# Kernel optimization log

Hardware: AMD Instinct MI355X
Metric: run time of the kernel (lower is better)

## Reference

```python
import jax, jax.numpy as jnp
import numpy as np

D_MODEL = 1024
H = 16
D_K = D_MODEL // H
B, S = 2, 2048
NEG = -1.0e9


def setup_inputs() -> dict:
    key = jax.random.key(0)
    ks = jax.random.split(key, 9)
    sc = 1.0 / np.sqrt(D_MODEL)
    x = jax.random.normal(ks[0], (B, S, D_MODEL), dtype=jnp.float32)
    mask = jnp.tril(jnp.ones((S, S), dtype=jnp.int32))[None, None]  # causal [1,1,S,S]
    Wq = jax.random.normal(ks[1], (D_MODEL, D_MODEL), jnp.float32) * sc
    bq = jnp.zeros((D_MODEL,), jnp.float32)
    Wk = jax.random.normal(ks[2], (D_MODEL, D_MODEL), jnp.float32) * sc
    bk = jnp.zeros((D_MODEL,), jnp.float32)
    Wv = jax.random.normal(ks[3], (D_MODEL, D_MODEL), jnp.float32) * sc
    bv = jnp.zeros((D_MODEL,), jnp.float32)
    Wo = jax.random.normal(ks[4], (D_MODEL, D_MODEL), jnp.float32) * sc
    bo = jnp.zeros((D_MODEL,), jnp.float32)
    return {"x": x, "mask": mask, "Wq": Wq, "bq": bq, "Wk": Wk, "bk": bk,
            "Wv": Wv, "bv": bv, "Wo": Wo, "bo": bo}


def reference(x, mask, Wq, bq, Wk, bk, Wv, bv, Wo, bo):
    Bx, Sx, _ = x.shape
    # QKV projections (nn.Linear: x @ W.T + b)
    q = (x @ Wq.T + bq).reshape(Bx, Sx, H, D_K).transpose(0, 2, 1, 3)  # [B,h,S,dk]
    k = (x @ Wk.T + bk).reshape(Bx, Sx, H, D_K).transpose(0, 2, 1, 3)
    v = (x @ Wv.T + bv).reshape(Bx, Sx, H, D_K).transpose(0, 2, 1, 3)
    scores = jnp.einsum('bhqd,bhkd->bhqk', q, k) / np.sqrt(D_K)  # [B,h,S,S]
    scores = jnp.where(mask == 0, NEG, scores)
    attn = jax.nn.softmax(scores, axis=-1)  # dropout p=0 -> identity
    out = jnp.einsum('bhqk,bhkd->bhqd', attn, v)
    out = out.transpose(0, 2, 1, 3).reshape(Bx, Sx, H * D_K)
    return out @ Wo.T + bo
```

## Files before the change

### kernel.cpp

```cpp
#include <hip/hip_runtime.h>
#include <hip/hip_bf16.h>

typedef __bf16 bf16;
typedef bf16 bf16x8 __attribute__((ext_vector_type(8)));
typedef bf16 bf16x4 __attribute__((ext_vector_type(4)));
typedef float f32x4 __attribute__((ext_vector_type(4)));
typedef float f32x16 __attribute__((ext_vector_type(16)));
typedef unsigned int u32;
typedef u32 u32x4 __attribute__((ext_vector_type(4)));

#define S_LEN 2048
#define DM 1024
#define NH 16
#define DK 64
#define MTOK 4096

__device__ __forceinline__ void gld16(const void* g, void* l) {
  __builtin_amdgcn_global_load_lds(
      (const __attribute__((address_space(1))) u32*)g,
      (__attribute__((address_space(3))) u32*)l, 16, 0, 0);
}

__device__ __forceinline__ u32 pkbf(float lo, float hi) {
  union { bf16 h[2]; u32 u; } c;
  c.h[0] = (bf16)lo; c.h[1] = (bf16)hi;
  return c.u;
}
__device__ __forceinline__ void plswap(u32& a, u32& b) {
  asm volatile("v_permlane32_swap_b32 %0, %1" : "+v"(a), "+v"(b));
}

__global__ __launch_bounds__(256) void cvt_all(
    const float* __restrict__ x, const float* __restrict__ wq, const float* __restrict__ wk,
    const float* __restrict__ wv, const float* __restrict__ wo,
    bf16* __restrict__ xb, bf16* __restrict__ wqb, bf16* __restrict__ wkb,
    bf16* __restrict__ wvb, bf16* __restrict__ wob) {
  const int i = blockIdx.x * blockDim.x + threadIdx.x;
  const int NX = (MTOK * DM) / 4;
  const int NW = (DM * DM) / 4;
  const float* src;
  bf16* dst;
  int off;
  if (i < NX) {
    src = x; dst = xb; off = i;
  } else {
    const int j = i - NX;
    const int w = j >> 18;
    off = j & (NW - 1);
    src = (w == 0) ? wq : (w == 1) ? wk : (w == 2) ? wv : wo;
    dst = (w == 0) ? wqb : (w == 1) ? wkb : (w == 2) ? wvb : wob;
  }
  f32x4 v = reinterpret_cast<const f32x4*>(src)[off];
  bf16x4 o;
  o[0] = (bf16)v[0]; o[1] = (bf16)v[1]; o[2] = (bf16)v[2]; o[3] = (bf16)v[3];
  reinterpret_cast<bf16x4*>(dst)[off] = o;
}

__global__ __launch_bounds__(256) void gemm_qkv(
    const bf16* __restrict__ A,
    const bf16* __restrict__ Wq, const bf16* __restrict__ Wk, const bf16* __restrict__ Wv,
    const float* __restrict__ Bq, const float* __restrict__ Bk, const float* __restrict__ Bv,
    bf16* __restrict__ Qo, bf16* __restrict__ Ko, bf16* __restrict__ Vt) {
  __shared__ char smem[65536];
  const int z = blockIdx.z;
  const bf16* W = (z == 0) ? Wq : (z == 1) ? Wk : Wv;
  const float* bias = (z == 0) ? Bq : (z == 1) ? Bk : Bv;
  const int m0 = blockIdx.y * 128;
  const int n0 = blockIdx.x * 128;
  const int tid = threadIdx.x;
  const int lane = tid & 63;
  const int wid = tid >> 6;
  const int wr = (wid >> 1) * 64, wc = (wid & 1) * 64;
  const int scb = 16 * ((lane & 7) ^ (lane >> 3));
  const int lr8 = lane >> 3;

  f32x4 acc[4][4] = {};

  auto STAGE = [&](int bi, int k0) {
#pragma unroll
    for (int c = 0; c < 4; ++c) {
      const int chunk = wid * 4 + c;
      const int row = chunk * 8 + lr8;
      gld16((const char*)A + ((size_t)(m0 + row) * DM + k0) * 2 + scb,
            smem + bi * 32768 + chunk * 1024);
      gld16((const char*)W + ((size_t)(n0 + row) * DM + k0) * 2 + scb,
            smem + bi * 32768 + 16384 + chunk * 1024);
    }
  };

  STAGE(0, 0);
  asm volatile("s_waitcnt vmcnt(0)" ::: "memory");
  __builtin_amdgcn_s_barrier();

  const int NK = DM / 64;
  for (int it = 0; it < NK; ++it) {
    if (it + 1 < NK) STAGE((it + 1) & 1, (it + 1) * 64);
    const char* As = smem + (it & 1) * 32768;
    const char* Bs = As + 16384;
#pragma unroll
    for (int kk = 0; kk < 2; ++kk) {
      bf16x8 af[4], bfr[4];
#pragma unroll
      for (int i = 0; i < 4; ++i) {
        const int ar = wr + i * 16 + (lane & 15);
        af[i] = *reinterpret_cast<const bf16x8*>(
            As + ar * 128 + ((kk * 64 + 16 * (lane >> 4)) ^ ((ar & 7) << 4)));
        const int br = wc + i * 16 + (lane & 15);
        bfr[i] = *reinterpret_cast<const bf16x8*>(
            Bs + br * 128 + ((kk * 64 + 16 * (lane >> 4)) ^ ((br & 7) << 4)));
      }
      __builtin_amdgcn_s_setprio(1);
#pragma unroll
      for (int i = 0; i < 4; ++i)
#pragma unroll
        for (int j = 0; j < 4; ++j)
          acc[i][j] = __builtin_amdgcn_mfma_f32_16x16x32_bf16(af[i], bfr[j], acc[i][j], 0, 0, 0);
      __builtin_amdgcn_s_setprio(0);
    }
    asm volatile("s_waitcnt vmcnt(0)" ::: "memory");
    __builtin_amdgcn_s_barrier();
  }

  const float QSC = 0.125f * 1.44269504089f;
  const int bIdx = m0 >> 11;
  const int r4 = (lane >> 4) * 4;
#pragma unroll
  for (int i = 0; i < 4; ++i) {
    const int mrow = m0 + wr + i * 16 + r4;
    const int srow = mrow & (S_LEN - 1);
#pragma unroll
    for (int j = 0; j < 4; ++j) {
      const int n = n0 + wc + j * 16 + (lane & 15);
      const int h = n >> 6, d = n & 63;
      const int bh = bIdx * NH + h;
      const float bs = bias[n];
      if (z == 0) {
#pragma unroll
        for (int r = 0; r < 4; ++r)
          Qo[((size_t)bh * S_LEN + srow + r) * DK + d] = (bf16)((acc[i][j][r] + bs) * QSC);
      } else if (z == 1) {
#pragma unroll
        for (int r = 0; r < 4; ++r)
          Ko[((size_t)bh * S_LEN + srow + r) * DK + d] = (bf16)(acc[i][j][r] + bs);
      } else {
        bf16x4 pk;
#pragma unroll
        for (int r = 0; r < 4; ++r) pk[r] = (bf16)(acc[i][j][r] + bs);
        *reinterpret_cast<bf16x4*>(&Vt[((size_t)bh * DK + d) * S_LEN + srow]) = pk;
      }
    }
  }
}

__global__ __launch_bounds__(256) void attn_fwd(
    const bf16* __restrict__ Q, const bf16* __restrict__ K,
    const bf16* __restrict__ Vt, bf16* __restrict__ O) {
  __shared__ char smem[49152];

  const int bid = blockIdx.x;
  const int qt = 15 - (bid >> 5);
  const int bh = bid & 31;
  const int tid = threadIdx.x, lane = tid & 63, wid = tid >> 6;
  const int q0 = qt * 128;
  const int scb = 16 * ((lane & 7) ^ (lane >> 3));
  const int l31 = lane & 31;
  const int hi = lane >> 5;
  const int qrow = q0 + wid * 32 + l31;
  const int swz = (l31 & 7) << 4;

  const bf16* qb = Q + ((size_t)bh * S_LEN + qrow) * DK;
  bf16x8 qf[4];
#pragma unroll
  for (int ks = 0; ks < 4; ++ks)
    qf[ks] = *reinterpret_cast<const bf16x8*>(qb + ks * 16 + 8 * hi);

  f32x16 o0 = {}, o1 = {};
  float m_r = -3.0e38f, l_r = 0.f;

  const int nt = 2 * (qt + 1);

  auto STAGE = [&](int bi, int t) {
    const int kv0 = t * 64;
#pragma unroll
    for (int c = 0; c < 2; ++c) {
      const int chunk = wid * 2 + c;
      const int row = chunk * 8 + (lane >> 3);
      gld16((const char*)K + ((size_t)(bh * S_LEN + kv0 + row)) * 128 + scb,
            smem + bi * 16384 + chunk * 1024);
      gld16((const char*)Vt + ((size_t)(bh * DK + row)) * (S_LEN * 2) + (size_t)kv0 * 2 + scb,
            smem + bi * 16384 + 8192 + chunk * 1024);
    }
  };

  STAGE(0, 0);

  for (int t = 0; t < nt; ++t) {
    const int kv0 = t * 64;
    if (t + 1 < nt) {
      STAGE((t + 1) % 3, t + 1);
      asm volatile("s_waitcnt vmcnt(4)" ::: "memory");
    } else {
      asm volatile("s_waitcnt vmcnt(0)" ::: "memory");
    }
    __builtin_amdgcn_s_barrier();
    asm volatile("" ::: "memory");
    const char* Kc = smem + (t % 3) * 16384;
    const char* Vc = Kc + 8192;

    f32x16 s0 = {}, s1 = {};
#pragma unroll
    for (int kt = 0; kt < 2; ++kt) {
      bf16x8 ka[4];
#pragma unroll
      for (int ks = 0; ks < 4; ++ks)
        ka[ks] = *reinterpret_cast<const bf16x8*>(
            Kc + (kt * 32 + l31) * 128 + ((ks * 32 + 16 * hi) ^ swz));
      f32x16& sd = kt ? s1 : s0;
      __builtin_amdgcn_s_setprio(1);
#pragma unroll
      for (int ks = 0; ks < 4; ++ks)
        sd = __builtin_amdgcn_mfma_f32_32x32x16_bf16(ka[ks], qf[ks], sd, 0, 0, 0);
      __builtin_amdgcn_s_setprio(0);
    }

    if (t >= nt - 2) {
#pragma unroll
      for (int r = 0; r < 16; ++r) {
        const int key0 = kv0 + (r & 3) + 8 * (r >> 2) + 4 * hi;
        if (key0 > qrow) s0[r] = -1.0e9f;
        if (key0 + 32 > qrow) s1[r] = -1.0e9f;
      }
    }

    float mx = s0[0];
#pragma unroll
    for (int r = 1; r < 16; ++r) mx = fmaxf(mx, s0[r]);
#pragma unroll
    for (int r = 0; r < 16; ++r) mx = fmaxf(mx, s1[r]);
    mx = fmaxf(mx, __shfl_xor(mx, 32));
    if (!__all(mx <= m_r + 8.f)) {
      const float nm = fmaxf(m_r, mx);
      const float sc = exp2f(m_r - nm);
      l_r *= sc;
      o0 *= sc;
      o1 *= sc;
      m_r = nm;
    }
    float rs = 0.f;
#pragma unroll
    for (int r = 0; r < 16; ++r) { s0[r] = exp2f(s0[r] - m_r); rs += s0[r]; }
#pragma unroll
    for (int r = 0; r < 16; ++r) { s1[r] = exp2f(s1[r] - m_r); rs += s1[r]; }
    rs += __shfl_xor(rs, 32);
    l_r += rs;

    bf16x8 pb[4];
#pragma unroll
    for (int kt = 0; kt < 2; ++kt) {
      const f32x16& p = kt ? s1 : s0;
#pragma unroll
      for (int s2 = 0; s2 < 2; ++s2) {
        u32 cA = pkbf(p[8 * s2 + 0], p[8 * s2 + 1]);
        u32 cB = pkbf(p[8 * s2 + 2], p[8 * s2 + 3]);
        u32 cC = pkbf(p[8 * s2 + 4], p[8 * s2 + 5]);
        u32 cD = pkbf(p[8 * s2 + 6], p[8 * s2 + 7]);
        plswap(cA, cC);
        plswap(cB, cD);
        u32x4 w;
        w[0] = cA; w[1] = cB; w[2] = cC; w[3] = cD;
        pb[kt * 2 + s2] = __builtin_bit_cast(bf16x8, w);
      }
    }

#pragma unroll
    for (int dt = 0; dt < 2; ++dt) {
      bf16x8 va[4];
#pragma unroll
      for (int ks = 0; ks < 4; ++ks)
        va[ks] = *reinterpret_cast<const bf16x8*>(
            Vc + (dt * 32 + l31) * 128 + ((ks * 32 + 16 * hi) ^ swz));
      f32x16& od = dt ? o1 : o0;
      __builtin_amdgcn_s_setprio(1);
#pragma unroll
      for (int ks = 0; ks < 4; ++ks)
        od = __builtin_amdgcn_mfma_f32_32x32x16_bf16(va[ks], pb[ks], od, 0, 0, 0);
      __builtin_amdgcn_s_setprio(0);
    }
  }

  const int b = bh >> 4, h = bh & 15;
  const float inv = 1.0f / l_r;
  bf16* obase = O + ((size_t)(b * S_LEN + qrow)) * DM + h * DK;
#pragma unroll
  for (int dt = 0; dt < 2; ++dt) {
    const f32x16& od = dt ? o1 : o0;
#pragma unroll
    for (int g = 0; g < 4; ++g) {
      bf16x4 pk4;
#pragma unroll
      for (int m = 0; m < 4; ++m) pk4[m] = (bf16)(od[4 * g + m] * inv);
      *reinterpret_cast<bf16x4*>(obase + dt * 32 + 8 * g + 4 * hi) = pk4;
    }
  }
}

__global__ __launch_bounds__(256) void gemm_out(
    const bf16* __restrict__ A, const bf16* __restrict__ W,
    const float* __restrict__ bias, float* __restrict__ C) {
  __shared__ char smem[65536];
  const int m0 = blockIdx.y * 128, n0 = blockIdx.x * 128;
  const int tid = threadIdx.x, lane = tid & 63, wid = tid >> 6;
  const int wr = (wid >> 1) * 64, wc = (wid & 1) * 64;
  const int scb = 16 * ((lane & 7) ^ (lane >> 3));
  const int lr8 = lane >> 3;
  f32x4 acc[4][4] = {};

  auto STAGE = [&](int bi, int k0) {
#pragma unroll
    for (int c = 0; c < 4; ++c) {
      const int chunk = wid * 4 + c;
      const int row = chunk * 8 + lr8;
      gld16((const char*)A + ((size_t)(m0 + row) * DM + k0) * 2 + scb,
            smem + bi * 32768 + chunk * 1024);
      gld16((const char*)W + ((size_t)(n0 + row) * DM + k0) * 2 + scb,
            smem + bi * 32768 + 16384 + chunk * 1024);
    }
  };

  STAGE(0, 0);
  asm volatile("s_waitcnt vmcnt(0)" ::: "memory");
  __builtin_amdgcn_s_barrier();

  const int NK = DM / 64;
  for (int it = 0; it < NK; ++it) {
    if (it + 1 < NK) STAGE((it + 1) & 1, (it + 1) * 64);
    const char* As = smem + (it & 1) * 32768;
    const char* Bs = As + 16384;
#pragma unroll
    for (int kk = 0; kk < 2; ++kk) {
      bf16x8 af[4], bfr[4];
#pragma unroll
      for (int i = 0; i < 4; ++i) {
        const int ar = wr + i * 16 + (lane & 15);
        af[i] = *reinterpret_cast<const bf16x8*>(
            As + ar * 128 + ((kk * 64 + 16 * (lane >> 4)) ^ ((ar & 7) << 4)));
        const int br = wc + i * 16 + (lane & 15);
        bfr[i] = *reinterpret_cast<const bf16x8*>(
            Bs + br * 128 + ((kk * 64 + 16 * (lane >> 4)) ^ ((br & 7) << 4)));
      }
      __builtin_amdgcn_s_setprio(1);
#pragma unroll
      for (int i = 0; i < 4; ++i)
#pragma unroll
        for (int j = 0; j < 4; ++j)
          acc[i][j] = __builtin_amdgcn_mfma_f32_16x16x32_bf16(af[i], bfr[j], acc[i][j], 0, 0, 0);
      __builtin_amdgcn_s_setprio(0);
    }
    asm volatile("s_waitcnt vmcnt(0)" ::: "memory");
    __builtin_amdgcn_s_barrier();
  }

  const int r4 = (lane >> 4) * 4;
#pragma unroll
  for (int i = 0; i < 4; ++i) {
    const int mrow = m0 + wr + i * 16 + r4;
#pragma unroll
    for (int j = 0; j < 4; ++j) {
      const int n = n0 + wc + j * 16 + (lane & 15);
      const float bs = bias[n];
#pragma unroll
      for (int r = 0; r < 4; ++r) C[(size_t)(mrow + r) * DM + n] = acc[i][j][r] + bs;
    }
  }
}

extern "C" void kernel_launch(void* const* d_in, const int* in_sizes, int n_in,
                              void* d_out, int out_size, void* d_ws, size_t ws_size,
                              hipStream_t stream) {
  const float* x = (const float*)d_in[0];
  const float* Wq = (const float*)d_in[2];
  const float* bq = (const float*)d_in[3];
  const float* Wk = (const float*)d_in[4];
  const float* bk = (const float*)d_in[5];
  const float* Wv = (const float*)d_in[6];
  const float* bv = (const float*)d_in[7];
  const float* Wo = (const float*)d_in[8];
  const float* bo = (const float*)d_in[9];

  char* ws = (char*)d_ws;
  bf16* xb  = (bf16*)(ws);
  bf16* wqb = (bf16*)(ws + (8u << 20));
  bf16* wkb = (bf16*)(ws + (10u << 20));
  bf16* wvb = (bf16*)(ws + (12u << 20));
  bf16* wob = (bf16*)(ws + (14u << 20));
  bf16* Qw  = (bf16*)(ws + (16u << 20));
  bf16* Kw  = (bf16*)(ws + (24u << 20));
  bf16* Vtw = (bf16*)(ws + (32u << 20));
  bf16* AO  = (bf16*)(ws + (40u << 20));

  cvt_all<<<8192, 256, 0, stream>>>(x, Wq, Wk, Wv, Wo, xb, wqb, wkb, wvb, wob);

  gemm_qkv<<<dim3(DM / 128, MTOK / 128, 3), 256, 0, stream>>>(
      xb, wqb, wkb, wvb, bq, bk, bv, Qw, Kw, Vtw);
  attn_fwd<<<dim3(512), 256, 0, stream>>>(Qw, Kw, Vtw, AO);
  gemm_out<<<dim3(DM / 128, MTOK / 128), 256, 0, stream>>>(AO, wob, bo, (float*)d_out);
}
```

Measured before the change: 118.6 us.

## Split attention KV range across two blocks and merge partial results

```diff
diff --git a/kernel.cpp b/kernel.cpp
--- a/kernel.cpp
+++ b/kernel.cpp
@@ -154,12 +154,17 @@
 
 __global__ __launch_bounds__(256) void attn_fwd(
     const bf16* __restrict__ Q, const bf16* __restrict__ K,
-    const bf16* __restrict__ Vt, bf16* __restrict__ O) {
+    const bf16* __restrict__ Vt,
+    bf16* __restrict__ O0p, bf16* __restrict__ O1p,
+    float* __restrict__ L0, float* __restrict__ M0,
+    float* __restrict__ L1, float* __restrict__ M1) {
   __shared__ char smem[49152];
 
   const int bid = blockIdx.x;
-  const int qt = 15 - (bid >> 5);
-  const int bh = bid & 31;
+  const int half = bid >> 9;
+  const int sub = bid & 511;
+  const int qt = 15 - (sub >> 5);
+  const int bh = sub & 31;
   const int tid = threadIdx.x, lane = tid & 63, wid = tid >> 6;
   const int q0 = qt * 128;
   const int scb = 16 * ((lane & 7) ^ (lane >> 3));
@@ -177,7 +182,9 @@
   f32x16 o0 = {}, o1 = {};
   float m_r = -3.0e38f, l_r = 0.f;
 
-  const int nt = 2 * (qt + 1);
+  const int t0 = half * (qt + 1);
+  const int t1 = t0 + qt + 1;
+  const int tdiag = 2 * qt;
 
   auto STAGE = [&](int bi, int t) {
     const int kv0 = t * 64;
@@ -192,11 +199,11 @@
     }
   };
 
-  STAGE(0, 0);
-
-  for (int t = 0; t < nt; ++t) {
+  STAGE(t0 % 3, t0);
+
+  for (int t = t0; t < t1; ++t) {
     const int kv0 = t * 64;
-    if (t + 1 < nt) {
+    if (t + 1 < t1) {
       STAGE((t + 1) % 3, t + 1);
       asm volatile("s_waitcnt vmcnt(4)" ::: "memory");
     } else {
@@ -223,7 +230,7 @@
       __builtin_amdgcn_s_setprio(0);
     }
 
-    if (t >= nt - 2) {
+    if (t >= tdiag) {
 #pragma unroll
       for (int r = 0; r < 16; ++r) {
         const int key0 = kv0 + (r & 3) + 8 * (r >> 2) + 4 * hi;
@@ -232,12 +239,14 @@
       }
     }
 
-    float mx = s0[0];
-#pragma unroll
-    for (int r = 1; r < 16; ++r) mx = fmaxf(mx, s0[r]);
-#pragma unroll
-    for (int r = 0; r < 16; ++r) mx = fmaxf(mx, s1[r]);
-    mx = fmaxf(mx, __shfl_xor(mx, 32));
+    float tmax[16];
+#pragma unroll
+    for (int r = 0; r < 16; ++r) tmax[r] = fmaxf(s0[r], s1[r]);
+#pragma unroll
+    for (int w = 8; w >= 1; w >>= 1)
+#pragma unroll
+      for (int r = 0; r < w; ++r) tmax[r] = fmaxf(tmax[r], tmax[r + w]);
+    const float mx = fmaxf(tmax[0], __shfl_xor(tmax[0], 32));
     if (!__all(mx <= m_r + 8.f)) {
       const float nm = fmaxf(m_r, mx);
       const float sc = exp2f(m_r - nm);
@@ -246,13 +255,18 @@
       o1 *= sc;
       m_r = nm;
     }
-    float rs = 0.f;
-#pragma unroll
-    for (int r = 0; r < 16; ++r) { s0[r] = exp2f(s0[r] - m_r); rs += s0[r]; }
-#pragma unroll
-    for (int r = 0; r < 16; ++r) { s1[r] = exp2f(s1[r] - m_r); rs += s1[r]; }
-    rs += __shfl_xor(rs, 32);
-    l_r += rs;
+    float ts[16];
+#pragma unroll
+    for (int r = 0; r < 16; ++r) {
+      s0[r] = exp2f(s0[r] - m_r);
+      s1[r] = exp2f(s1[r] - m_r);
+      ts[r] = s0[r] + s1[r];
+    }
+#pragma unroll
+    for (int w = 8; w >= 1; w >>= 1)
+#pragma unroll
+      for (int r = 0; r < w; ++r) ts[r] += ts[r + w];
+    l_r += ts[0] + __shfl_xor(ts[0], 32);
 
     bf16x8 pb[4];
 #pragma unroll
@@ -289,8 +303,8 @@
   }
 
   const int b = bh >> 4, h = bh & 15;
-  const float inv = 1.0f / l_r;
-  bf16* obase = O + ((size_t)(b * S_LEN + qrow)) * DM + h * DK;
+  bf16* Opart = half ? O1p : O0p;
+  bf16* obase = Opart + ((size_t)(b * S_LEN + qrow)) * DM + h * DK;
 #pragma unroll
   for (int dt = 0; dt < 2; ++dt) {
     const f32x16& od = dt ? o1 : o0;
@@ -298,10 +312,38 @@
     for (int g = 0; g < 4; ++g) {
       bf16x4 pk4;
 #pragma unroll
-      for (int m = 0; m < 4; ++m) pk4[m] = (bf16)(od[4 * g + m] * inv);
+      for (int m = 0; m < 4; ++m) pk4[m] = (bf16)od[4 * g + m];
       *reinterpret_cast<bf16x4*>(obase + dt * 32 + 8 * g + 4 * hi) = pk4;
     }
   }
+  const int lmi = bh * S_LEN + qrow;
+  if (half) { L1[lmi] = l_r; M1[lmi] = m_r; }
+  else      { L0[lmi] = l_r; M0[lmi] = m_r; }
+}
+
+__global__ __launch_bounds__(256) void attn_merge(
+    const bf16* __restrict__ O0, const bf16* __restrict__ O1,
+    const float* __restrict__ L0, const float* __restrict__ M0,
+    const float* __restrict__ L1, const float* __restrict__ M1,
+    bf16* __restrict__ AO) {
+  const int i = blockIdx.x * blockDim.x + threadIdx.x;
+  const int e = i * 8;
+  const int row = e >> 10;
+  const int b = row >> 11, s = row & 2047;
+  const int h = (e >> 6) & 15;
+  const int lmi = (b * NH + h) * S_LEN + s;
+  const float m0 = M0[lmi], m1 = M1[lmi];
+  const float m = fmaxf(m0, m1);
+  const float a0 = exp2f(m0 - m), a1 = exp2f(m1 - m);
+  const float inv = 1.0f / (a0 * L0[lmi] + a1 * L1[lmi]);
+  const float f0 = a0 * inv, f1 = a1 * inv;
+  bf16x8 v0 = *reinterpret_cast<const bf16x8*>(O0 + e);
+  bf16x8 v1 = *reinterpret_cast<const bf16x8*>(O1 + e);
+  bf16x8 o;
+#pragma unroll
+  for (int j = 0; j < 8; ++j)
+    o[j] = (bf16)(f0 * (float)v0[j] + f1 * (float)v1[j]);
+  *reinterpret_cast<bf16x8*>(AO + e) = o;
 }
 
 __global__ __launch_bounds__(256) void gemm_out(
@@ -398,10 +440,18 @@
   bf16* Vtw = (bf16*)(ws + (32u << 20));
   bf16* AO  = (bf16*)(ws + (40u << 20));
 
+  bf16* O0p = (bf16*)(ws);
+  bf16* O1p = AO;
+  float* L0 = (float*)(ws + (8u << 20));
+  float* M0 = (float*)(ws + (8u << 20) + 262144);
+  float* L1 = (float*)(ws + (8u << 20) + 524288);
+  float* M1 = (float*)(ws + (8u << 20) + 786432);
+
   cvt_all<<<8192, 256, 0, stream>>>(x, Wq, Wk, Wv, Wo, xb, wqb, wkb, wvb, wob);
 
   gemm_qkv<<<dim3(DM / 128, MTOK / 128, 3), 256, 0, stream>>>(
       xb, wqb, wkb, wvb, bq, bk, bv, Qw, Kw, Vtw);
-  attn_fwd<<<dim3(512), 256, 0, stream>>>(Qw, Kw, Vtw, AO);
+  attn_fwd<<<dim3(1024), 256, 0, stream>>>(Qw, Kw, Vtw, O0p, O1p, L0, M0, L1, M1);
+  attn_merge<<<dim3(2048), 256, 0, stream>>>(O0p, O1p, L0, M0, L1, M1, AO);
   gemm_out<<<dim3(DM / 128, MTOK / 128), 256, 0, stream>>>(AO, wob, bo, (float*)d_out);
 }
```

Measured after the change: 120.4 us. About the same (+1.5%).

## Make attention wave-independent with direct global K/V loads; fix GEMM prefetch wait placement

Applied to the files above, without the earlier changes.

```diff
diff --git a/kernel.cpp b/kernel.cpp
--- a/kernel.cpp
+++ b/kernel.cpp
@@ -89,12 +89,17 @@
   };
 
   STAGE(0, 0);
-  asm volatile("s_waitcnt vmcnt(0)" ::: "memory");
-  __builtin_amdgcn_s_barrier();
 
   const int NK = DM / 64;
   for (int it = 0; it < NK; ++it) {
-    if (it + 1 < NK) STAGE((it + 1) & 1, (it + 1) * 64);
+    if (it + 1 < NK) {
+      STAGE((it + 1) & 1, (it + 1) * 64);
+      asm volatile("s_waitcnt vmcnt(8)" ::: "memory");
+    } else {
+      asm volatile("s_waitcnt vmcnt(0)" ::: "memory");
+    }
+    __builtin_amdgcn_s_barrier();
+    asm volatile("" ::: "memory");
     const char* As = smem + (it & 1) * 32768;
     const char* Bs = As + 16384;
 #pragma unroll
@@ -117,7 +122,7 @@
           acc[i][j] = __builtin_amdgcn_mfma_f32_16x16x32_bf16(af[i], bfr[j], acc[i][j], 0, 0, 0);
       __builtin_amdgcn_s_setprio(0);
     }
-    asm volatile("s_waitcnt vmcnt(0)" ::: "memory");
+    asm volatile("" ::: "memory");
     __builtin_amdgcn_s_barrier();
   }
 
@@ -155,75 +160,55 @@
 __global__ __launch_bounds__(256) void attn_fwd(
     const bf16* __restrict__ Q, const bf16* __restrict__ K,
     const bf16* __restrict__ Vt, bf16* __restrict__ O) {
-  __shared__ char smem[49152];
-
-  const int bid = blockIdx.x;
-  const int qt = 15 - (bid >> 5);
-  const int bh = bid & 31;
   const int tid = threadIdx.x, lane = tid & 63, wid = tid >> 6;
-  const int q0 = qt * 128;
-  const int scb = 16 * ((lane & 7) ^ (lane >> 3));
+  const int widx = blockIdx.x * 4 + wid;
+  const int qb = 63 - (widx >> 5);
+  const int bh = widx & 31;
   const int l31 = lane & 31;
   const int hi = lane >> 5;
-  const int qrow = q0 + wid * 32 + l31;
-  const int swz = (l31 & 7) << 4;
-
-  const bf16* qb = Q + ((size_t)bh * S_LEN + qrow) * DK;
+  const int qrow = qb * 32 + l31;
+  const int nt = (qb >> 1) + 1;
+
+  const bf16* qp = Q + ((size_t)bh * S_LEN + qrow) * DK;
   bf16x8 qf[4];
 #pragma unroll
   for (int ks = 0; ks < 4; ++ks)
-    qf[ks] = *reinterpret_cast<const bf16x8*>(qb + ks * 16 + 8 * hi);
+    qf[ks] = *reinterpret_cast<const bf16x8*>(qp + ks * 16 + 8 * hi);
+
+  const bf16* Kb = K + (size_t)bh * S_LEN * DK;
+  const bf16* Vb = Vt + (size_t)bh * DK * S_LEN;
 
   f32x16 o0 = {}, o1 = {};
   float m_r = -3.0e38f, l_r = 0.f;
 
-  const int nt = 2 * (qt + 1);
-
-  auto STAGE = [&](int bi, int t) {
-    const int kv0 = t * 64;
-#pragma unroll
-    for (int c = 0; c < 2; ++c) {
-      const int chunk = wid * 2 + c;
-      const int row = chunk * 8 + (lane >> 3);
-      gld16((const char*)K + ((size_t)(bh * S_LEN + kv0 + row)) * 128 + scb,
-            smem + bi * 16384 + chunk * 1024);
-      gld16((const char*)Vt + ((size_t)(bh * DK + row)) * (S_LEN * 2) + (size_t)kv0 * 2 + scb,
-            smem + bi * 16384 + 8192 + chunk * 1024);
-    }
-  };
-
-  STAGE(0, 0);
-
   for (int t = 0; t < nt; ++t) {
     const int kv0 = t * 64;
-    if (t + 1 < nt) {
-      STAGE((t + 1) % 3, t + 1);
-      asm volatile("s_waitcnt vmcnt(4)" ::: "memory");
-    } else {
-      asm volatile("s_waitcnt vmcnt(0)" ::: "memory");
-    }
-    __builtin_amdgcn_s_barrier();
-    asm volatile("" ::: "memory");
-    const char* Kc = smem + (t % 3) * 16384;
-    const char* Vc = Kc + 8192;
+
+    bf16x8 ka0[4], ka1[4];
+#pragma unroll
+    for (int ks = 0; ks < 4; ++ks) {
+      ka0[ks] = *reinterpret_cast<const bf16x8*>(
+          Kb + (size_t)(kv0 + l31) * DK + ks * 16 + 8 * hi);
+      ka1[ks] = *reinterpret_cast<const bf16x8*>(
+          Kb + (size_t)(kv0 + 32 + l31) * DK + ks * 16 + 8 * hi);
+    }
+    bf16x8 va0[4], va1[4];
+#pragma unroll
+    for (int ks = 0; ks < 4; ++ks) {
+      va0[ks] = *reinterpret_cast<const bf16x8*>(
+          Vb + (size_t)(0 + l31) * S_LEN + kv0 + ks * 16 + 8 * hi);
+      va1[ks] = *reinterpret_cast<const bf16x8*>(
+          Vb + (size_t)(32 + l31) * S_LEN + kv0 + ks * 16 + 8 * hi);
+    }
 
     f32x16 s0 = {}, s1 = {};
 #pragma unroll
-    for (int kt = 0; kt < 2; ++kt) {
-      bf16x8 ka[4];
-#pragma unroll
-      for (int ks = 0; ks < 4; ++ks)
-        ka[ks] = *reinterpret_cast<const bf16x8*>(
-            Kc + (kt * 32 + l31) * 128 + ((ks * 32 + 16 * hi) ^ swz));
-      f32x16& sd = kt ? s1 : s0;
-      __builtin_amdgcn_s_setprio(1);
-#pragma unroll
-      for (int ks = 0; ks < 4; ++ks)
-        sd = __builtin_amdgcn_mfma_f32_32x32x16_bf16(ka[ks], qf[ks], sd, 0, 0, 0);
-      __builtin_amdgcn_s_setprio(0);
-    }
-
-    if (t >= nt - 2) {
+    for (int ks = 0; ks < 4; ++ks) {
+      s0 = __builtin_amdgcn_mfma_f32_32x32x16_bf16(ka0[ks], qf[ks], s0, 0, 0, 0);
+      s1 = __builtin_amdgcn_mfma_f32_32x32x16_bf16(ka1[ks], qf[ks], s1, 0, 0, 0);
+    }
+
+    if (t == nt - 1) {
 #pragma unroll
       for (int r = 0; r < 16; ++r) {
         const int key0 = kv0 + (r & 3) + 8 * (r >> 2) + 4 * hi;
@@ -232,12 +217,14 @@
       }
     }
 
-    float mx = s0[0];
-#pragma unroll
-    for (int r = 1; r < 16; ++r) mx = fmaxf(mx, s0[r]);
-#pragma unroll
-    for (int r = 0; r < 16; ++r) mx = fmaxf(mx, s1[r]);
-    mx = fmaxf(mx, __shfl_xor(mx, 32));
+    float tmax[16];
+#pragma unroll
+    for (int r = 0; r < 16; ++r) tmax[r] = fmaxf(s0[r], s1[r]);
+#pragma unroll
+    for (int w = 8; w >= 1; w >>= 1)
+#pragma unroll
+      for (int r = 0; r < w; ++r) tmax[r] = fmaxf(tmax[r], tmax[r + w]);
+    const float mx = fmaxf(tmax[0], __shfl_xor(tmax[0], 32));
     if (!__all(mx <= m_r + 8.f)) {
       const float nm = fmaxf(m_r, mx);
       const float sc = exp2f(m_r - nm);
@@ -246,13 +233,18 @@
       o1 *= sc;
       m_r = nm;
     }
-    float rs = 0.f;
-#pragma unroll
-    for (int r = 0; r < 16; ++r) { s0[r] = exp2f(s0[r] - m_r); rs += s0[r]; }
-#pragma unroll
-    for (int r = 0; r < 16; ++r) { s1[r] = exp2f(s1[r] - m_r); rs += s1[r]; }
-    rs += __shfl_xor(rs, 32);
-    l_r += rs;
+    float ts[16];
+#pragma unroll
+    for (int r = 0; r < 16; ++r) {
+      s0[r] = exp2f(s0[r] - m_r);
+      s1[r] = exp2f(s1[r] - m_r);
+      ts[r] = s0[r] + s1[r];
+    }
+#pragma unroll
+    for (int w = 8; w >= 1; w >>= 1)
+#pragma unroll
+      for (int r = 0; r < w; ++r) ts[r] += ts[r + w];
+    l_r += ts[0] + __shfl_xor(ts[0], 32);
 
     bf16x8 pb[4];
 #pragma unroll
@@ -273,18 +265,9 @@
     }
 
 #pragma unroll
-    for (int dt = 0; dt < 2; ++dt) {
-      bf16x8 va[4];
-#pragma unroll
-      for (int ks = 0; ks < 4; ++ks)
-        va[ks] = *reinterpret_cast<const bf16x8*>(
-            Vc + (dt * 32 + l31) * 128 + ((ks * 32 + 16 * hi) ^ swz));
-      f32x16& od = dt ? o1 : o0;
-      __builtin_amdgcn_s_setprio(1);
-#pragma unroll
-      for (int ks = 0; ks < 4; ++ks)
-        od = __builtin_amdgcn_mfma_f32_32x32x16_bf16(va[ks], pb[ks], od, 0, 0, 0);
-      __builtin_amdgcn_s_setprio(0);
+    for (int ks = 0; ks < 4; ++ks) {
+      o0 = __builtin_amdgcn_mfma_f32_32x32x16_bf16(va0[ks], pb[ks], o0, 0, 0, 0);
+      o1 = __builtin_amdgcn_mfma_f32_32x32x16_bf16(va1[ks], pb[ks], o1, 0, 0, 0);
     }
   }
 
@@ -328,12 +311,17 @@
   };
 
   STAGE(0, 0);
-  asm volatile("s_waitcnt vmcnt(0)" ::: "memory");
-  __builtin_amdgcn_s_barrier();
 
   const int NK = DM / 64;
   for (int it = 0; it < NK; ++it) {
-    if (it + 1 < NK) STAGE((it + 1) & 1, (it + 1) * 64);
+    if (it + 1 < NK) {
+      STAGE((it + 1) & 1, (it + 1) * 64);
+      asm volatile("s_waitcnt vmcnt(8)" ::: "memory");
+    } else {
+      asm volatile("s_waitcnt vmcnt(0)" ::: "memory");
+    }
+    __builtin_amdgcn_s_barrier();
+    asm volatile("" ::: "memory");
     const char* As = smem + (it & 1) * 32768;
     const char* Bs = As + 16384;
 #pragma unroll
@@ -356,7 +344,7 @@
           acc[i][j] = __builtin_amdgcn_mfma_f32_16x16x32_bf16(af[i], bfr[j], acc[i][j], 0, 0, 0);
       __builtin_amdgcn_s_setprio(0);
     }
-    asm volatile("s_waitcnt vmcnt(0)" ::: "memory");
+    asm volatile("" ::: "memory");
     __builtin_amdgcn_s_barrier();
   }
 
```

Result: slower. 152.2 us (+28.4%).
